# Kernel optimization log

Hardware: AMD Instinct MI355X
Metric: run time of the kernel (lower is better)

## Reference

```python
import jax, jax.numpy as jnp
import numpy as np
from functools import partial

# Module hyperparameters (from init_kwargs)
T, C_IN, H, W_DIM = 128, 16, 64, 64
C_OUT, KH, KW = 64, 3, 3
PAD = ((1, 1), (1, 1))  # (top,bottom),(left,right) -> symmetric here
STRIDES = (1, 1)
F_V_THRESH = 8.0
F_V_THRESH_LOW = -1.0
F_V_RESET = 0.0
# fVSubtract is None -> reset-to-value branch


def setup_inputs() -> dict:
    key = jax.random.key(0)
    kx, kw, kb = jax.random.split(key, 3)
    x = jax.random.uniform(kx, (T, C_IN, H, W_DIM), dtype=jnp.float32)
    fan_in = C_IN * KH * KW
    bound = 1.0 / np.sqrt(fan_in)
    W = jax.random.uniform(kw, (C_OUT, C_IN, KH, KW), dtype=jnp.float32,
                           minval=-bound, maxval=bound)
    b = jax.random.uniform(kb, (C_OUT,), dtype=jnp.float32,
                           minval=-bound, maxval=bound)
    return {"x": x, "W": W, "b": b}


def _spiking_conv(x, W, b):
    # conv over all timesteps at once (time is the conv batch dim): [T, C_out, H, W]
    conv_out = jax.lax.conv_general_dilated(
        x, W, window_strides=STRIDES, padding=PAD,
        dimension_numbers=("NCHW", "OIHW", "NCHW"))
    conv_out = conv_out + b[None, :, None, None]

    def step(state, conv_t):
        state = state + conv_t
        spikes = (state >= F_V_THRESH).astype(conv_t.dtype)
        # reset-to-value branch (fVSubtract is None)
        state = spikes * F_V_RESET + state * (1.0 - spikes)
        # nn.Threshold(v, v): x if x > v else v
        state = jnp.where(state > F_V_THRESH_LOW, state, F_V_THRESH_LOW)
        return state, spikes

    init_state = jnp.zeros(conv_out.shape[1:], dtype=conv_out.dtype)
    _, num_spikes = jax.lax.scan(step, init_state, conv_out)
    return num_spikes  # [T, C_out, H, W] float (0/1)


def reference(x, W, b):
    return _spiking_conv(x, W, b)
```

## Files before the change

### kernel.cpp

```cpp
#include <hip/hip_runtime.h>

#define T_STEPS 128
#define CIN     16
#define HH      64
#define WW      64
#define COUT    64
#define HWSZ    (HH * WW)
#define CHW     (COUT * HWSZ)
#define XCHW    (CIN * HWSZ)

#define TILE    32
#define HALO    34
#define LSTR    36
#define PLANE   (HALO * LSTR)
#define NST     (CIN * HALO * HALO)
#define WBLK    40

__global__ void transpose_w(const float* __restrict__ W, float* __restrict__ Wtr) {
    int e = blockIdx.x * 256 + threadIdx.x;
    if (e >= COUT * CIN * 9) return;
    int co = e / (CIN * 9);
    int r  = e - co * (CIN * 9);
    int ci = r / 9;
    int k  = r - ci * 9;
    Wtr[((co >> 2) * CIN + ci) * WBLK + (co & 3) * 9 + k] = W[e];
}

__global__ __launch_bounds__(512, 4)
void spiking_conv_pass1(const float* __restrict__ x, const float* __restrict__ Wtr,
                        const float* __restrict__ b, float* __restrict__ out) {
    __shared__ float xs[CIN * PLANE];

    const int tid = threadIdx.x;
    const int t   = blockIdx.y;
    const int h0  = (blockIdx.x >> 1) * TILE;
    const int w0  = (blockIdx.x & 1) * TILE;
    const int coh = blockIdx.z;

    const float* xt = x + t * XCHW;
    {
        float vbuf[19]; int ibuf[19];
#pragma unroll
        for (int k = 0; k < 18; ++k) {
            unsigned e = tid + k * 512;
            unsigned ci = e / (HALO * HALO);
            unsigned rem = e - ci * (HALO * HALO);
            unsigned r  = rem / HALO;
            unsigned c  = rem - r * HALO;
            int gh = h0 - 1 + (int)r;
            int gw = w0 - 1 + (int)c;
            bool inb = (unsigned)gh < HH && (unsigned)gw < WW;
            vbuf[k] = inb ? xt[ci * HWSZ + gh * WW + gw] : 0.f;
            ibuf[k] = ci * PLANE + r * LSTR + c;
        }
#pragma unroll
        for (int k = 0; k < 18; ++k) xs[ibuf[k]] = vbuf[k];
#pragma unroll
        for (int k = 0; k < 19; ++k) {
            unsigned e = tid + (18 + k) * 512;
            unsigned ci = e / (HALO * HALO);
            unsigned rem = e - ci * (HALO * HALO);
            unsigned r  = rem / HALO;
            unsigned c  = rem - r * HALO;
            int gh = h0 - 1 + (int)r;
            int gw = w0 - 1 + (int)c;
            bool inb = e < NST && (unsigned)gh < HH && (unsigned)gw < WW;
            vbuf[k] = inb ? xt[ci * HWSZ + gh * WW + gw] : 0.f;
            ibuf[k] = (e < NST) ? (int)(ci * PLANE + r * LSTR + c) : -1;
        }
#pragma unroll
        for (int k = 0; k < 19; ++k)
            if (ibuf[k] >= 0) xs[ibuf[k]] = vbuf[k];
    }
    __syncthreads();

    const int cog = __builtin_amdgcn_readfirstlane(tid >> 8);
    const int sp  = tid & 255;
    const int pr0 = sp >> 3;
    const int pc0 = (sp & 7) * 4;
    float* outt = out + t * CHW;

    float acc[16][4];
#pragma unroll
    for (int j = 0; j < 16; ++j)
#pragma unroll
        for (int p = 0; p < 4; ++p) acc[j][p] = 0.f;

#pragma unroll 1
    for (int ci = 0; ci < CIN; ++ci) {
        float xv[3][6];
#pragma unroll
        for (int dr = 0; dr < 3; ++dr) {
            const float* row = &xs[ci * PLANE + (pr0 + dr) * LSTR + pc0];
            float4 a  = *(const float4*)row;
            float2 c2 = *(const float2*)(row + 4);
            xv[dr][0] = a.x;  xv[dr][1] = a.y;
            xv[dr][2] = a.z;  xv[dr][3] = a.w;
            xv[dr][4] = c2.x; xv[dr][5] = c2.y;
        }
#pragma unroll
        for (int g = 0; g < 4; ++g) {
            const int g4 = coh * 8 + cog * 4 + g;
            const float* wb = Wtr + (g4 * CIN + ci) * WBLK;
            float w[36];
#pragma unroll
            for (int i = 0; i < 36; ++i) w[i] = wb[i];
#pragma unroll
            for (int jj = 0; jj < 4; ++jj)
#pragma unroll
                for (int ky = 0; ky < 3; ++ky)
#pragma unroll
                    for (int kx = 0; kx < 3; ++kx) {
                        const float wv = w[jj * 9 + ky * 3 + kx];
#pragma unroll
                        for (int p = 0; p < 4; ++p)
                            acc[g * 4 + jj][p] += wv * xv[ky][kx + p];
                    }
        }
    }

#pragma unroll
    for (int g = 0; g < 4; ++g)
#pragma unroll
        for (int jj = 0; jj < 4; ++jj) {
            const int co = coh * 32 + cog * 16 + g * 4 + jj;
            const float bias = b[co];
            float4 o;
            o.x = acc[g * 4 + jj][0] + bias;
            o.y = acc[g * 4 + jj][1] + bias;
            o.z = acc[g * 4 + jj][2] + bias;
            o.w = acc[g * 4 + jj][3] + bias;
            *(float4*)&outt[co * HWSZ + (h0 + pr0) * WW + (w0 + pc0)] = o;
        }
}

__global__ __launch_bounds__(256)
void spiking_scan_pass2(float* __restrict__ io) {
    const int idx = blockIdx.x * 256 + threadIdx.x;
    float4* p = (float4*)io + idx;
    float sx = 0.f, sy = 0.f, sz = 0.f, sw = 0.f;
    float4 v[8], nv[8];
#pragma unroll
    for (int i = 0; i < 8; ++i) v[i] = p[(size_t)i * (CHW / 4)];
#pragma unroll 1
    for (int tb = 0; tb < 15; ++tb) {
#pragma unroll
        for (int i = 0; i < 8; ++i) nv[i] = p[(size_t)((tb + 1) * 8 + i) * (CHW / 4)];
#pragma unroll
        for (int i = 0; i < 8; ++i) {
            float4 o;
            sx += v[i].x; bool a0 = (sx >= 8.0f); o.x = a0 ? 1.f : 0.f; sx = a0 ? 0.f : sx; sx = fmaxf(sx, -1.f);
            sy += v[i].y; bool a1 = (sy >= 8.0f); o.y = a1 ? 1.f : 0.f; sy = a1 ? 0.f : sy; sy = fmaxf(sy, -1.f);
            sz += v[i].z; bool a2 = (sz >= 8.0f); o.z = a2 ? 1.f : 0.f; sz = a2 ? 0.f : sz; sz = fmaxf(sz, -1.f);
            sw += v[i].w; bool a3 = (sw >= 8.0f); o.w = a3 ? 1.f : 0.f; sw = a3 ? 0.f : sw; sw = fmaxf(sw, -1.f);
            p[(size_t)(tb * 8 + i) * (CHW / 4)] = o;
        }
#pragma unroll
        for (int i = 0; i < 8; ++i) v[i] = nv[i];
    }
#pragma unroll
    for (int i = 0; i < 8; ++i) {
        float4 o;
        sx += v[i].x; bool a0 = (sx >= 8.0f); o.x = a0 ? 1.f : 0.f; sx = a0 ? 0.f : sx; sx = fmaxf(sx, -1.f);
        sy += v[i].y; bool a1 = (sy >= 8.0f); o.y = a1 ? 1.f : 0.f; sy = a1 ? 0.f : sy; sy = fmaxf(sy, -1.f);
        sz += v[i].z; bool a2 = (sz >= 8.0f); o.z = a2 ? 1.f : 0.f; sz = a2 ? 0.f : sz; sz = fmaxf(sz, -1.f);
        sw += v[i].w; bool a3 = (sw >= 8.0f); o.w = a3 ? 1.f : 0.f; sw = a3 ? 0.f : sw; sw = fmaxf(sw, -1.f);
        p[(size_t)(120 + i) * (CHW / 4)] = o;
    }
}

extern "C" void kernel_launch(void* const* d_in, const int* in_sizes, int n_in,
                              void* d_out, int out_size, void* d_ws, size_t ws_size,
                              hipStream_t stream) {
    const float* x = (const float*)d_in[0];
    const float* W = (const float*)d_in[1];
    const float* b = (const float*)d_in[2];
    float* out = (float*)d_out;
    float* Wtr = (float*)d_ws;

    transpose_w<<<36, 256, 0, stream>>>(W, Wtr);

    dim3 g1(4, 128, 2);
    spiking_conv_pass1<<<g1, 512, 0, stream>>>(x, Wtr, b, out);

    spiking_scan_pass2<<<(CHW / 4) / 256, 256, 0, stream>>>(out);
}
```

Baseline: 263.9 us.

## Stage scan pass through LDS with async global-to-LDS loads and remap conv grid

The scan pass now has each block load a 128-position by 128-timestep tile into shared memory using direct global-to-LDS loads. Only 128 of 256 threads then run the sequential threshold scan over time in shared memory, and the block writes the tile back with float2 stores. This replaces the earlier per-thread float4 streaming with register prefetch, aiming for more loads in flight and better coalescing. The conv grid is also remapped so the two output-channel halves of a tile run in adjacent blocks, which should improve L2 reuse of the input tile. The cost is 64KB of LDS per scan block, which limits occupancy, and a serial scan that uses only half the threads.

```diff
diff --git a/kernel.cpp b/kernel.cpp
--- a/kernel.cpp
+++ b/kernel.cpp
@@ -31,11 +31,12 @@
                         const float* __restrict__ b, float* __restrict__ out) {
     __shared__ float xs[CIN * PLANE];
 
-    const int tid = threadIdx.x;
-    const int t   = blockIdx.y;
-    const int h0  = (blockIdx.x >> 1) * TILE;
-    const int w0  = (blockIdx.x & 1) * TILE;
-    const int coh = blockIdx.z;
+    const int tid  = threadIdx.x;
+    const int t    = blockIdx.y;
+    const int coh  = blockIdx.x & 1;
+    const int tile = blockIdx.x >> 1;
+    const int h0   = (tile >> 1) * TILE;
+    const int w0   = (tile & 1) * TILE;
 
     const float* xt = x + t * XCHW;
     {
@@ -134,38 +135,51 @@
         }
 }
 
+#define SCH 128
+
+__device__ __forceinline__ void gl_lds_4(const float* g, float* l) {
+    __builtin_amdgcn_global_load_lds(
+        (const __attribute__((address_space(1))) void*)g,
+        (__attribute__((address_space(3))) void*)l, 4, 0, 0);
+}
+
 __global__ __launch_bounds__(256)
 void spiking_scan_pass2(float* __restrict__ io) {
-    const int idx = blockIdx.x * 256 + threadIdx.x;
-    float4* p = (float4*)io + idx;
-    float sx = 0.f, sy = 0.f, sz = 0.f, sw = 0.f;
-    float4 v[8], nv[8];
-#pragma unroll
-    for (int i = 0; i < 8; ++i) v[i] = p[(size_t)i * (CHW / 4)];
-#pragma unroll 1
-    for (int tb = 0; tb < 15; ++tb) {
-#pragma unroll
-        for (int i = 0; i < 8; ++i) nv[i] = p[(size_t)((tb + 1) * 8 + i) * (CHW / 4)];
-#pragma unroll
-        for (int i = 0; i < 8; ++i) {
-            float4 o;
-            sx += v[i].x; bool a0 = (sx >= 8.0f); o.x = a0 ? 1.f : 0.f; sx = a0 ? 0.f : sx; sx = fmaxf(sx, -1.f);
-            sy += v[i].y; bool a1 = (sy >= 8.0f); o.y = a1 ? 1.f : 0.f; sy = a1 ? 0.f : sy; sy = fmaxf(sy, -1.f);
-            sz += v[i].z; bool a2 = (sz >= 8.0f); o.z = a2 ? 1.f : 0.f; sz = a2 ? 0.f : sz; sz = fmaxf(sz, -1.f);
-            sw += v[i].w; bool a3 = (sw >= 8.0f); o.w = a3 ? 1.f : 0.f; sw = a3 ? 0.f : sw; sw = fmaxf(sw, -1.f);
-            p[(size_t)(tb * 8 + i) * (CHW / 4)] = o;
-        }
-#pragma unroll
-        for (int i = 0; i < 8; ++i) v[i] = nv[i];
-    }
-#pragma unroll
-    for (int i = 0; i < 8; ++i) {
-        float4 o;
-        sx += v[i].x; bool a0 = (sx >= 8.0f); o.x = a0 ? 1.f : 0.f; sx = a0 ? 0.f : sx; sx = fmaxf(sx, -1.f);
-        sy += v[i].y; bool a1 = (sy >= 8.0f); o.y = a1 ? 1.f : 0.f; sy = a1 ? 0.f : sy; sy = fmaxf(sy, -1.f);
-        sz += v[i].z; bool a2 = (sz >= 8.0f); o.z = a2 ? 1.f : 0.f; sz = a2 ? 0.f : sz; sz = fmaxf(sz, -1.f);
-        sw += v[i].w; bool a3 = (sw >= 8.0f); o.w = a3 ? 1.f : 0.f; sw = a3 ? 0.f : sw; sw = fmaxf(sw, -1.f);
-        p[(size_t)(120 + i) * (CHW / 4)] = o;
+    __shared__ float tile[T_STEPS * SCH];
+    const int tid = threadIdx.x;
+    const int wv  = tid >> 6;
+    const int ln  = tid & 63;
+    const int s0  = blockIdx.x * SCH;
+
+#pragma unroll
+    for (int i = 0; i < 32; ++i) {
+        const int t = wv * 32 + i;
+        const float* g = io + t * CHW + s0;
+        float* l = &tile[t * SCH];
+        gl_lds_4(g + ln, l);
+        gl_lds_4(g + 64 + ln, l + 64);
+    }
+    __syncthreads();
+
+    if (tid < SCH) {
+        float s = 0.f;
+#pragma unroll 8
+        for (int t = 0; t < T_STEPS; ++t) {
+            float v = tile[t * SCH + tid];
+            s += v;
+            const bool sp = (s >= 8.0f);
+            tile[t * SCH + tid] = sp ? 1.0f : 0.0f;
+            s = sp ? 0.0f : s;
+            s = fmaxf(s, -1.0f);
+        }
+    }
+    __syncthreads();
+
+#pragma unroll
+    for (int i = 0; i < 32; ++i) {
+        const int t = wv * 32 + i;
+        float2 v = *(const float2*)&tile[t * SCH + ln * 2];
+        *(float2*)(io + t * CHW + s0 + ln * 2) = v;
     }
 }
 
@@ -180,8 +194,8 @@
 
     transpose_w<<<36, 256, 0, stream>>>(W, Wtr);
 
-    dim3 g1(4, 128, 2);
+    dim3 g1(8, 128);
     spiking_conv_pass1<<<g1, 512, 0, stream>>>(x, Wtr, b, out);
 
-    spiking_scan_pass2<<<(CHW / 4) / 256, 256, 0, stream>>>(out);
-}
+    spiking_scan_pass2<<<CHW / SCH, 256, 0, stream>>>(out);
+}
```

Result: no change. 267.4 us (+1.3%).
